# Kernel optimization log

Hardware: AMD Instinct MI355X
Metric: run time of the kernel (lower is better)

The kernel has to match this reference:

```python
import jax
import jax.numpy as jnp
import numpy as np

VOCAB = 100      # len(vocab); embedding table has VOCAB+1 rows
EMBED = 10
MID = 100
SEQ = 550
OUT = 1


def setup_inputs() -> dict:
    key = jax.random.key(0)
    ks = jax.random.split(key, 8)
    s_ih = 1.0 / np.sqrt(MID)
    return {
        "x": jax.random.randint(ks[0], (SEQ,), 0, VOCAB + 1),
        "hidden": jnp.zeros((1, 1, MID), dtype=jnp.float32),
        "embed_table": jax.random.normal(ks[1], (VOCAB + 1, EMBED), dtype=jnp.float32),
        "w_ih": jax.random.uniform(ks[2], (3 * MID, EMBED), minval=-s_ih, maxval=s_ih, dtype=jnp.float32),
        "w_hh": jax.random.uniform(ks[3], (3 * MID, MID), minval=-s_ih, maxval=s_ih, dtype=jnp.float32),
        "b_ih": jax.random.uniform(ks[4], (3 * MID,), minval=-s_ih, maxval=s_ih, dtype=jnp.float32),
        "b_hh": jax.random.uniform(ks[5], (3 * MID,), minval=-s_ih, maxval=s_ih, dtype=jnp.float32),
        "fc_w": jax.random.uniform(ks[6], (OUT, MID), minval=-s_ih, maxval=s_ih, dtype=jnp.float32),
        "fc_b": jax.random.uniform(ks[7], (OUT,), minval=-s_ih, maxval=s_ih, dtype=jnp.float32),
    }


def reference(x, hidden, embed_table, w_ih, w_hh, b_ih, b_hh, fc_w, fc_b):
    # embedding lookup: [SEQ, EMBED]
    emb = embed_table[x]
    # precompute input-side gate projections for all timesteps: [SEQ, 3*MID]
    gi_all = emb @ w_ih.T + b_ih
    h0 = hidden[0, 0]  # [MID]

    def step(h, gi):
        gh = w_hh @ h + b_hh                      # [3*MID]
        i_r, i_z, i_n = jnp.split(gi, 3)
        h_r, h_z, h_n = jnp.split(gh, 3)
        r = jax.nn.sigmoid(i_r + h_r)
        z = jax.nn.sigmoid(i_z + h_z)
        n = jnp.tanh(i_n + r * h_n)
        h_new = (1.0 - z) * n + z * h
        return h_new, None

    h_final, _ = jax.lax.scan(step, h0, gi_all)   # h_final: [MID]
    out = jax.nn.sigmoid(jax.nn.relu(h_final) @ fc_w.T + fc_b)  # [OUT]
    return out.reshape(1, 1, OUT)
```

## Files before the change

### kernel.cpp

```cpp
#include <hip/hip_runtime.h>

#define SEQ 550
#define MID 100
#define TPB 256

typedef _Float16 half2_t __attribute__((ext_vector_type(2)));

union H2I { int i; half2_t h; ushort2 u2; };

__device__ __forceinline__ float fdot2(half2_t a, half2_t b, float c) {
    return __builtin_amdgcn_fdot2(a, b, c, false);
}
__device__ __forceinline__ float sigm(float x) { return 1.0f / (1.0f + __expf(-x)); }
__device__ __forceinline__ float tanh_f(float x) { return 1.0f - 2.0f / (__expf(2.0f * x) + 1.0f); }
__device__ __forceinline__ half2_t i2h(int v) { H2I u; u.i = v; return u.h; }

__device__ __forceinline__ float pair_sum(float x) {
    int yi = __builtin_amdgcn_update_dpp(0, __float_as_int(x), 0xB1, 0xF, 0xF, true);
    return x + __int_as_float(yi);
}

__global__ __launch_bounds__(TPB, 1) void gru_fused(
    const int*   __restrict__ x,
    const float* __restrict__ hidden,
    const float* __restrict__ embed,
    const float* __restrict__ w_ih,
    const float* __restrict__ w_hh,
    const float* __restrict__ b_ih,
    const float* __restrict__ b_hh,
    const float* __restrict__ fc_w,
    const float* __restrict__ fc_b,
    float*       __restrict__ out)
{
    __shared__ __align__(16) ushort seqbuf[SEQ * 16];
    __shared__ __align__(16) int hbuf[128];
    __shared__ float partial[MID];

    const int  tid = threadIdx.x;
    const bool act = tid < 2 * MID;
    const int  u   = tid >> 1;
    const int  p   = tid & 1;
    const int  hidx = (u < 50) ? u : u + 14;

    for (int i = tid; i < SEQ * 10; i += TPB) {
        int t = i / 10;
        int k = i - 10 * t;
        H2I c; c.h = half2_t{(_Float16)embed[x[t] * 10 + k], (_Float16)0.0f};
        seqbuf[t * 16 + (k < 6 ? k : k + 2)] = c.u2.x;
    }
    for (int i = tid; i < SEQ; i += TPB)
        *(int*)(seqbuf + i * 16 + 12) = 0;

    half2_t whh[3][25];
    half2_t wihr[3][3];
    float b0 = 0.f, b1 = 0.f, b2 = 0.f, b3 = 0.f;
    float hreg = 0.f, fcw = 0.f;

    if (act) {
        #pragma unroll
        for (int r = 0; r < 3; r++) {
            const int row = r * MID + u;
            const float2* wr = (const float2*)(w_hh + row * MID) + 25 * p;
            #pragma unroll
            for (int k = 0; k < 25; k++) {
                float2 f = wr[k];
                whh[r][k] = half2_t{(_Float16)f.x, (_Float16)f.y};
            }
            const float* wi = w_ih + row * 10 + 6 * p;
            wihr[r][0] = half2_t{(_Float16)wi[0], (_Float16)wi[1]};
            wihr[r][1] = half2_t{(_Float16)wi[2], (_Float16)wi[3]};
            if (p == 0) wihr[r][2] = half2_t{(_Float16)wi[4], (_Float16)wi[5]};
            else        wihr[r][2] = half2_t{(_Float16)0.0f, (_Float16)0.0f};
        }
        if (p == 0) {
            b0 = b_ih[u]           + b_hh[u];
            b1 = b_ih[MID + u]     + b_hh[MID + u];
            b2 = b_ih[2 * MID + u];
            b3 = b_hh[2 * MID + u];
        }
        hreg = hidden[u];
        fcw  = fc_w[u];
        if (p == 0) ((_Float16*)hbuf)[hidx] = (_Float16)hreg;
    }
    float fcb = (tid == 0) ? fc_b[0] : 0.0f;

    __syncthreads();

    #pragma unroll 1
    for (int t = 0; t < SEQ; t++) {
        if (act) {
            const int   rbase = ((t & 1) << 8) + (p << 7);
            const int4* hp4   = (const int4*)((const char*)hbuf + rbase);
            int4 q0 = hp4[0], q1 = hp4[1], q2 = hp4[2], q3 = hp4[3], q4 = hp4[4], q5 = hp4[5];
            int  qe = ((const int*)hp4)[24];
            int4 ev = *(const int4*)(seqbuf + t * 16 + p * 8);

            half2_t hh[25];
            hh[0]=i2h(q0.x);  hh[1]=i2h(q0.y);  hh[2]=i2h(q0.z);  hh[3]=i2h(q0.w);
            hh[4]=i2h(q1.x);  hh[5]=i2h(q1.y);  hh[6]=i2h(q1.z);  hh[7]=i2h(q1.w);
            hh[8]=i2h(q2.x);  hh[9]=i2h(q2.y);  hh[10]=i2h(q2.z); hh[11]=i2h(q2.w);
            hh[12]=i2h(q3.x); hh[13]=i2h(q3.y); hh[14]=i2h(q3.z); hh[15]=i2h(q3.w);
            hh[16]=i2h(q4.x); hh[17]=i2h(q4.y); hh[18]=i2h(q4.z); hh[19]=i2h(q4.w);
            hh[20]=i2h(q5.x); hh[21]=i2h(q5.y); hh[22]=i2h(q5.z); hh[23]=i2h(q5.w);
            hh[24]=i2h(qe);

            float s0 = b0, s1 = b1, s2 = b2, s3 = b3;
            #pragma unroll
            for (int k = 0; k < 25; k++) {
                s0 = fdot2(whh[0][k], hh[k], s0);
                s1 = fdot2(whh[1][k], hh[k], s1);
                s3 = fdot2(whh[2][k], hh[k], s3);
            }
            half2_t e0 = i2h(ev.x), e1 = i2h(ev.y), e2 = i2h(ev.z);
            s0 = fdot2(wihr[0][0], e0, s0); s0 = fdot2(wihr[0][1], e1, s0); s0 = fdot2(wihr[0][2], e2, s0);
            s1 = fdot2(wihr[1][0], e0, s1); s1 = fdot2(wihr[1][1], e1, s1); s1 = fdot2(wihr[1][2], e2, s1);
            s2 = fdot2(wihr[2][0], e0, s2); s2 = fdot2(wihr[2][1], e1, s2); s2 = fdot2(wihr[2][2], e2, s2);

            float ar  = pair_sum(s0);
            float az  = pair_sum(s1);
            float gin = pair_sum(s2);
            float ghn = pair_sum(s3);

            float r = sigm(ar);
            float z = sigm(az);
            float n = tanh_f(gin + r * ghn);
            hreg = n + z * (hreg - n);
            if (p == 0)
                ((_Float16*)hbuf)[(((t & 1) ^ 1) << 7) + hidx] = (_Float16)hreg;
        }
        __syncthreads();
    }

    if (act && p == 0) partial[u] = fmaxf(hreg, 0.0f) * fcw;
    __syncthreads();
    if (tid == 0) {
        float s = fcb;
        const float4* pp = (const float4*)partial;
        #pragma unroll
        for (int k = 0; k < 25; k++) {
            float4 f = pp[k];
            s += (f.x + f.y) + (f.z + f.w);
        }
        out[0] = sigm(s);
    }
}

extern "C" void kernel_launch(void* const* d_in, const int* in_sizes, int n_in,
                              void* d_out, int out_size, void* d_ws, size_t ws_size,
                              hipStream_t stream) {
    const int*   x      = (const int*)  d_in[0];
    const float* hidden = (const float*)d_in[1];
    const float* embed  = (const float*)d_in[2];
    const float* w_ih   = (const float*)d_in[3];
    const float* w_hh   = (const float*)d_in[4];
    const float* b_ih   = (const float*)d_in[5];
    const float* b_hh   = (const float*)d_in[6];
    const float* fc_w   = (const float*)d_in[7];
    const float* fc_b   = (const float*)d_in[8];
    float*       out    = (float*)d_out;

    gru_fused<<<1, TPB, 0, stream>>>(x, hidden, embed, w_ih, w_hh,
                                     b_ih, b_hh, fc_w, fc_b, out);
}
```

Measured before the change: 294.7 us.

## Rewrite GRU recurrence as single-wavefront MFMA matvec with bpermute state broadcast

Shrinks the block to one 64-lane wavefront and computes the hidden-to-hidden and input projections with 16x16x32 fp16 MFMA instructions, keeping weights resident in AGPR/VGPR registers. The hidden state is broadcast across lanes via ds_bpermute instead of through shared memory with a block-wide barrier each step. Gate results go through a small LDS buffer and each lane then updates one or two hidden units. The aim is to remove per-step __syncthreads and the long scalar fdot2 chains. In exchange it adds MFMA latency and many bpermute ops to the serial critical path.

```diff
diff --git a/kernel.cpp b/kernel.cpp
--- a/kernel.cpp
+++ b/kernel.cpp
@@ -2,11 +2,16 @@
 
 #define SEQ 550
 #define MID 100
-#define TPB 256
+#define TPB 64
 
 typedef _Float16 half2_t __attribute__((ext_vector_type(2)));
-
-union H2I { int i; half2_t h; ushort2 u2; };
+typedef _Float16 half8_t __attribute__((ext_vector_type(8)));
+typedef __fp16  fp16x2  __attribute__((ext_vector_type(2)));
+typedef float f32x4 __attribute__((ext_vector_type(4)));
+
+union H2I { int i; half2_t h; };
+union H8X { half8_t h8; half2_t h2[4]; int4 i4; };
+union PKC { fp16x2 p; half2_t h; };
 
 __device__ __forceinline__ float fdot2(half2_t a, half2_t b, float c) {
     return __builtin_amdgcn_fdot2(a, b, c, false);
@@ -14,13 +19,21 @@
 __device__ __forceinline__ float sigm(float x) { return 1.0f / (1.0f + __expf(-x)); }
 __device__ __forceinline__ float tanh_f(float x) { return 1.0f - 2.0f / (__expf(2.0f * x) + 1.0f); }
 __device__ __forceinline__ half2_t i2h(int v) { H2I u; u.i = v; return u.h; }
-
-__device__ __forceinline__ float pair_sum(float x) {
-    int yi = __builtin_amdgcn_update_dpp(0, __float_as_int(x), 0xB1, 0xF, 0xF, true);
-    return x + __int_as_float(yi);
-}
-
-__global__ __launch_bounds__(TPB, 1) void gru_fused(
+__device__ __forceinline__ float pullf(int idx, float v) {
+    return __int_as_float(__builtin_amdgcn_ds_bpermute(idx, __float_as_int(v)));
+}
+__device__ __forceinline__ half2_t pk2(float a, float b) {
+    PKC u; u.p = __builtin_amdgcn_cvt_pkrtz(a, b); return u.h;
+}
+__device__ __forceinline__ half8_t zero8() {
+    return half8_t{(_Float16)0.f, (_Float16)0.f, (_Float16)0.f, (_Float16)0.f,
+                   (_Float16)0.f, (_Float16)0.f, (_Float16)0.f, (_Float16)0.f};
+}
+
+
+__global__ __launch_bounds__(TPB, 1)
+__attribute__((amdgpu_waves_per_eu(1, 1)))
+void gru_fused(
     const int*   __restrict__ x,
     const float* __restrict__ hidden,
     const float* __restrict__ embed,
@@ -32,117 +45,207 @@
     const float* __restrict__ fc_b,
     float*       __restrict__ out)
 {
-    __shared__ __align__(16) ushort seqbuf[SEQ * 16];
-    __shared__ __align__(16) int hbuf[128];
-    __shared__ float partial[MID];
-
-    const int  tid = threadIdx.x;
-    const bool act = tid < 2 * MID;
-    const int  u   = tid >> 1;
-    const int  p   = tid & 1;
-    const int  hidx = (u < 50) ? u : u + 14;
-
-    for (int i = tid; i < SEQ * 10; i += TPB) {
-        int t = i / 10;
-        int k = i - 10 * t;
-        H2I c; c.h = half2_t{(_Float16)embed[x[t] * 10 + k], (_Float16)0.0f};
-        seqbuf[t * 16 + (k < 6 ? k : k + 2)] = c.u2.x;
-    }
-    for (int i = tid; i < SEQ; i += TPB)
-        *(int*)(seqbuf + i * 16 + 12) = 0;
-
-    half2_t whh[3][25];
-    half2_t wihr[3][3];
-    float b0 = 0.f, b1 = 0.f, b2 = 0.f, b3 = 0.f;
-    float hreg = 0.f, fcw = 0.f;
-
-    if (act) {
+    __shared__ __align__(16) int seqbuf[SEQ * 16 + 16];
+    __shared__ __align__(16) int gates[400];
+
+    const int  l  = threadIdx.x;
+    const int  m  = l & 15;
+    const int  g  = l >> 4;
+    const bool m0 = (m == 0);
+
+    for (int i = l; i < SEQ * 16 + 16; i += TPB) seqbuf[i] = 0;
+    for (int i = l; i < SEQ * 5; i += TPB) {
+        int t = i / 5, j = i - 5 * t;
+        float2 f = *(const float2*)(embed + x[t] * 10 + 2 * j);
+        H2I c; c.h = half2_t{(_Float16)f.x, (_Float16)f.y};
+        seqbuf[t * 16 + j] = c.i;
+    }
+
+    half8_t ahh[19][3];
+    #pragma unroll
+    for (int tt = 0; tt < 19; tt++) {
+        int row = 0; bool val = true;
+        if (tt < 6)       row = tt * 16 + m;
+        else if (tt < 12) row = 100 + (tt - 6) * 16 + m;
+        else if (tt < 18) row = 200 + (tt - 12) * 16 + m;
+        else {
+            if (m < 4)       row = 96 + m;
+            else if (m < 8)  row = 196 + (m - 4);
+            else if (m < 12) row = 296 + (m - 8);
+            else             val = false;
+        }
         #pragma unroll
-        for (int r = 0; r < 3; r++) {
-            const int row = r * MID + u;
-            const float2* wr = (const float2*)(w_hh + row * MID) + 25 * p;
-            #pragma unroll
-            for (int k = 0; k < 25; k++) {
-                float2 f = wr[k];
-                whh[r][k] = half2_t{(_Float16)f.x, (_Float16)f.y};
+        for (int s = 0; s < 3; s++) {
+            half8_t a = zero8();
+            if (val) {
+                const float* p = w_hh + row * MID + 32 * s + 8 * g;
+                float4 f0 = *(const float4*)p;
+                float4 f1 = *(const float4*)(p + 4);
+                a = half8_t{(_Float16)f0.x, (_Float16)f0.y, (_Float16)f0.z, (_Float16)f0.w,
+                            (_Float16)f1.x, (_Float16)f1.y, (_Float16)f1.z, (_Float16)f1.w};
             }
-            const float* wi = w_ih + row * 10 + 6 * p;
-            wihr[r][0] = half2_t{(_Float16)wi[0], (_Float16)wi[1]};
-            wihr[r][1] = half2_t{(_Float16)wi[2], (_Float16)wi[3]};
-            if (p == 0) wihr[r][2] = half2_t{(_Float16)wi[4], (_Float16)wi[5]};
-            else        wihr[r][2] = half2_t{(_Float16)0.0f, (_Float16)0.0f};
-        }
-        if (p == 0) {
-            b0 = b_ih[u]           + b_hh[u];
-            b1 = b_ih[MID + u]     + b_hh[MID + u];
-            b2 = b_ih[2 * MID + u];
-            b3 = b_hh[2 * MID + u];
-        }
-        hreg = hidden[u];
-        fcw  = fc_w[u];
-        if (p == 0) ((_Float16*)hbuf)[hidx] = (_Float16)hreg;
-    }
-    float fcb = (tid == 0) ? fc_b[0] : 0.0f;
-
-    __syncthreads();
+            ahh[tt][s] = a;
+        }
+    }
+
+    half8_t aih[13];
+    #pragma unroll
+    for (int q = 0; q < 13; q++) {
+        int row = 0; bool val = true;
+        if (q < 6)       row = q * 16 + m;
+        else if (q < 12) row = 100 + (q - 6) * 16 + m;
+        else {
+            if (m < 4)      row = 96 + m;
+            else if (m < 8) row = 196 + (m - 4);
+            else            val = false;
+        }
+        half8_t a = zero8();
+        if (val) {
+            const float* p = w_ih + row * 10;
+            if (g == 0) {
+                float2 c0 = *(const float2*)(p);
+                float2 c1 = *(const float2*)(p + 2);
+                float2 c2 = *(const float2*)(p + 4);
+                float2 c3 = *(const float2*)(p + 6);
+                a = half8_t{(_Float16)c0.x, (_Float16)c0.y, (_Float16)c1.x, (_Float16)c1.y,
+                            (_Float16)c2.x, (_Float16)c2.y, (_Float16)c3.x, (_Float16)c3.y};
+            } else if (g == 1) {
+                float2 c = *(const float2*)(p + 8);
+                a[0] = (_Float16)c.x; a[1] = (_Float16)c.y;
+            }
+        }
+        aih[q] = a;
+    }
+
+    #pragma unroll
+    for (int tt = 0; tt < 19; tt++)
+        asm volatile("" : "+a"(ahh[tt][0]), "+a"(ahh[tt][1]), "+a"(ahh[tt][2]));
+    #pragma unroll
+    for (int q = 0; q < 13; q++)
+        asm volatile("" : "+v"(aih[q]));
+
+    const int u1 = l;
+    const int u2 = (l < 36) ? 64 + l : 99;
+
+    half2_t w96r1[2], w96z1[2], w96n1[2], w96r2[2], w96z2[2], w96n2[2];
+    {
+        float4 f;
+        f = *(const float4*)(w_hh + u1 * MID + 96);
+        w96r1[0] = half2_t{(_Float16)f.x, (_Float16)f.y}; w96r1[1] = half2_t{(_Float16)f.z, (_Float16)f.w};
+        f = *(const float4*)(w_hh + (MID + u1) * MID + 96);
+        w96z1[0] = half2_t{(_Float16)f.x, (_Float16)f.y}; w96z1[1] = half2_t{(_Float16)f.z, (_Float16)f.w};
+        f = *(const float4*)(w_hh + (2 * MID + u1) * MID + 96);
+        w96n1[0] = half2_t{(_Float16)f.x, (_Float16)f.y}; w96n1[1] = half2_t{(_Float16)f.z, (_Float16)f.w};
+        f = *(const float4*)(w_hh + u2 * MID + 96);
+        w96r2[0] = half2_t{(_Float16)f.x, (_Float16)f.y}; w96r2[1] = half2_t{(_Float16)f.z, (_Float16)f.w};
+        f = *(const float4*)(w_hh + (MID + u2) * MID + 96);
+        w96z2[0] = half2_t{(_Float16)f.x, (_Float16)f.y}; w96z2[1] = half2_t{(_Float16)f.z, (_Float16)f.w};
+        f = *(const float4*)(w_hh + (2 * MID + u2) * MID + 96);
+        w96n2[0] = half2_t{(_Float16)f.x, (_Float16)f.y}; w96n2[1] = half2_t{(_Float16)f.z, (_Float16)f.w};
+    }
+    half2_t win1[5], win2[5];
+    #pragma unroll
+    for (int k = 0; k < 5; k++) {
+        float2 a = *(const float2*)(w_ih + (2 * MID + u1) * 10 + 2 * k);
+        float2 b = *(const float2*)(w_ih + (2 * MID + u2) * 10 + 2 * k);
+        win1[k] = half2_t{(_Float16)a.x, (_Float16)a.y};
+        win2[k] = half2_t{(_Float16)b.x, (_Float16)b.y};
+    }
+    const float br1  = b_ih[u1] + b_hh[u1];
+    const float bz1  = b_ih[MID + u1] + b_hh[MID + u1];
+    const float bin1 = b_ih[2 * MID + u1];
+    const float bhn1 = b_hh[2 * MID + u1];
+    const float br2  = b_ih[u2] + b_hh[u2];
+    const float bz2  = b_ih[MID + u2] + b_hh[MID + u2];
+    const float bin2 = b_ih[2 * MID + u2];
+    const float bhn2 = b_hh[2 * MID + u2];
+
+    float h1 = hidden[u1];
+    float h2 = hidden[u2];
+    const float fw1 = fc_w[u1];
+    const float fw2 = fc_w[u2];
+
+    int idxA[8], idxB[8];
+    #pragma unroll
+    for (int j = 0; j < 8; j++) { idxA[j] = (8 * g + j) * 4; idxB[j] = idxA[j] + 128; }
+
+    const f32x4 zf = {0.f, 0.f, 0.f, 0.f};
+    const float* gf = (const float*)gates;
+    int soff = 0;
 
     #pragma unroll 1
     for (int t = 0; t < SEQ; t++) {
-        if (act) {
-            const int   rbase = ((t & 1) << 8) + (p << 7);
-            const int4* hp4   = (const int4*)((const char*)hbuf + rbase);
-            int4 q0 = hp4[0], q1 = hp4[1], q2 = hp4[2], q3 = hp4[3], q4 = hp4[4], q5 = hp4[5];
-            int  qe = ((const int*)hp4)[24];
-            int4 ev = *(const int4*)(seqbuf + t * 16 + p * 8);
-
-            half2_t hh[25];
-            hh[0]=i2h(q0.x);  hh[1]=i2h(q0.y);  hh[2]=i2h(q0.z);  hh[3]=i2h(q0.w);
-            hh[4]=i2h(q1.x);  hh[5]=i2h(q1.y);  hh[6]=i2h(q1.z);  hh[7]=i2h(q1.w);
-            hh[8]=i2h(q2.x);  hh[9]=i2h(q2.y);  hh[10]=i2h(q2.z); hh[11]=i2h(q2.w);
-            hh[12]=i2h(q3.x); hh[13]=i2h(q3.y); hh[14]=i2h(q3.z); hh[15]=i2h(q3.w);
-            hh[16]=i2h(q4.x); hh[17]=i2h(q4.y); hh[18]=i2h(q4.z); hh[19]=i2h(q4.w);
-            hh[20]=i2h(q5.x); hh[21]=i2h(q5.y); hh[22]=i2h(q5.z); hh[23]=i2h(q5.w);
-            hh[24]=i2h(qe);
-
-            float s0 = b0, s1 = b1, s2 = b2, s3 = b3;
-            #pragma unroll
-            for (int k = 0; k < 25; k++) {
-                s0 = fdot2(whh[0][k], hh[k], s0);
-                s1 = fdot2(whh[1][k], hh[k], s1);
-                s3 = fdot2(whh[2][k], hh[k], s3);
+        H8X be; be.i4 = *(const int4*)(seqbuf + soff + 4 * g);
+        int4 e03 = *(const int4*)(seqbuf + soff);
+        int  e4w = seqbuf[soff + 4];
+
+        H8X b0, b1, b2;
+        #pragma unroll
+        for (int j = 0; j < 4; j++) {
+            b0.h2[j] = pk2(pullf(idxA[2 * j], h1), pullf(idxA[2 * j + 1], h1));
+            b1.h2[j] = pk2(pullf(idxB[2 * j], h1), pullf(idxB[2 * j + 1], h1));
+            b2.h2[j] = pk2(pullf(idxA[2 * j], h2), pullf(idxA[2 * j + 1], h2));
+        }
+        half2_t tv0 = pk2(pullf(128, h2), pullf(132, h2));
+        half2_t tv1 = pk2(pullf(136, h2), pullf(140, h2));
+
+        #pragma unroll
+        for (int tt = 0; tt < 19; tt++) {
+            f32x4 d;
+            if (tt < 12)
+                d = __builtin_amdgcn_mfma_f32_16x16x32_f16(aih[tt], be.h8, zf, 0, 0, 0);
+            else if (tt == 18)
+                d = __builtin_amdgcn_mfma_f32_16x16x32_f16(aih[12], be.h8, zf, 0, 0, 0);
+            else
+                d = zf;
+            d = __builtin_amdgcn_mfma_f32_16x16x32_f16(ahh[tt][0], b0.h8, d, 0, 0, 0);
+            d = __builtin_amdgcn_mfma_f32_16x16x32_f16(ahh[tt][1], b1.h8, d, 0, 0, 0);
+            d = __builtin_amdgcn_mfma_f32_16x16x32_f16(ahh[tt][2], b2.h8, d, 0, 0, 0);
+            if (m0) {
+                int boff;
+                if (tt < 6)       boff = tt * 16 + 4 * g;
+                else if (tt < 12) boff = 100 + (tt - 6) * 16 + 4 * g;
+                else if (tt < 18) boff = 200 + (tt - 12) * 16 + 4 * g;
+                else              boff = (g == 0) ? 96 : (g == 1) ? 196 : (g == 2) ? 296 : 384;
+                *(f32x4*)(gates + boff) = d;
             }
-            half2_t e0 = i2h(ev.x), e1 = i2h(ev.y), e2 = i2h(ev.z);
-            s0 = fdot2(wihr[0][0], e0, s0); s0 = fdot2(wihr[0][1], e1, s0); s0 = fdot2(wihr[0][2], e2, s0);
-            s1 = fdot2(wihr[1][0], e0, s1); s1 = fdot2(wihr[1][1], e1, s1); s1 = fdot2(wihr[1][2], e2, s1);
-            s2 = fdot2(wihr[2][0], e0, s2); s2 = fdot2(wihr[2][1], e1, s2); s2 = fdot2(wihr[2][2], e2, s2);
-
-            float ar  = pair_sum(s0);
-            float az  = pair_sum(s1);
-            float gin = pair_sum(s2);
-            float ghn = pair_sum(s3);
-
-            float r = sigm(ar);
-            float z = sigm(az);
-            float n = tanh_f(gin + r * ghn);
-            hreg = n + z * (hreg - n);
-            if (p == 0)
-                ((_Float16*)hbuf)[(((t & 1) ^ 1) << 7) + hidx] = (_Float16)hreg;
-        }
-        __syncthreads();
-    }
-
-    if (act && p == 0) partial[u] = fmaxf(hreg, 0.0f) * fcw;
-    __syncthreads();
-    if (tid == 0) {
-        float s = fcb;
-        const float4* pp = (const float4*)partial;
-        #pragma unroll
-        for (int k = 0; k < 25; k++) {
-            float4 f = pp[k];
-            s += (f.x + f.y) + (f.z + f.w);
-        }
-        out[0] = sigm(s);
-    }
+        }
+
+        float gr1 = gf[u1], gz1 = gf[100 + u1], gn1 = gf[200 + u1];
+        float gr2 = gf[u2], gz2 = gf[100 + u2], gn2 = gf[200 + u2];
+
+        half2_t ev0 = i2h(e03.x), ev1 = i2h(e03.y), ev2 = i2h(e03.z), ev3 = i2h(e03.w), ev4 = i2h(e4w);
+
+        float ar1 = br1;  ar1 = fdot2(w96r1[0], tv0, ar1); ar1 = fdot2(w96r1[1], tv1, ar1); ar1 += gr1;
+        float az1 = bz1;  az1 = fdot2(w96z1[0], tv0, az1); az1 = fdot2(w96z1[1], tv1, az1); az1 += gz1;
+        float gh1 = bhn1; gh1 = fdot2(w96n1[0], tv0, gh1); gh1 = fdot2(w96n1[1], tv1, gh1); gh1 += gn1;
+        float gi1 = bin1;
+        gi1 = fdot2(win1[0], ev0, gi1); gi1 = fdot2(win1[1], ev1, gi1); gi1 = fdot2(win1[2], ev2, gi1);
+        gi1 = fdot2(win1[3], ev3, gi1); gi1 = fdot2(win1[4], ev4, gi1);
+
+        float ar2 = br2;  ar2 = fdot2(w96r2[0], tv0, ar2); ar2 = fdot2(w96r2[1], tv1, ar2); ar2 += gr2;
+        float az2 = bz2;  az2 = fdot2(w96z2[0], tv0, az2); az2 = fdot2(w96z2[1], tv1, az2); az2 += gz2;
+        float gh2 = bhn2; gh2 = fdot2(w96n2[0], tv0, gh2); gh2 = fdot2(w96n2[1], tv1, gh2); gh2 += gn2;
+        float gi2 = bin2;
+        gi2 = fdot2(win2[0], ev0, gi2); gi2 = fdot2(win2[1], ev1, gi2); gi2 = fdot2(win2[2], ev2, gi2);
+        gi2 = fdot2(win2[3], ev3, gi2); gi2 = fdot2(win2[4], ev4, gi2);
+
+        float r1 = sigm(ar1), z1 = sigm(az1);
+        float n1 = tanh_f(gi1 + r1 * gh1);
+        h1 = n1 + z1 * (h1 - n1);
+
+        float r2 = sigm(ar2), z2 = sigm(az2);
+        float n2 = tanh_f(gi2 + r2 * gh2);
+        float h2n = n2 + z2 * (h2 - n2);
+        h2 = (l < 36) ? h2n : h2;
+
+        soff += 16;
+    }
+
+    float acc = fmaxf(h1, 0.f) * fw1 + ((l < 36) ? fmaxf(h2, 0.f) * fw2 : 0.f);
+    #pragma unroll
+    for (int k = 32; k >= 1; k >>= 1) acc += __shfl_xor(acc, k, 64);
+    if (l == 0) out[0] = sigm(acc + fc_b[0]);
 }
 
 extern "C" void kernel_launch(void* const* d_in, const int* in_sizes, int n_in,
```

After: 818.9 us. 178% more time.

## Assign one hidden unit per lane across two waves, removing pair reduction

Applied to the files above, without the earlier changes.

The GRU step is reorganised so each active lane owns a full hidden unit and holds its whole 100-wide weight rows in registers, 150 packed half2 values. The block shrinks from 256 to 128 threads, two waves each covering 50 units. This removes the cross-lane DPP pair-sum and halves the number of waves taking part in the per-step barrier. The hidden state is now written as packed half2 pairs using a DPP neighbour pull, and the dot products are split into two accumulator chains to shorten dependency latency. The trade-off is doubled per-lane FMA work and heavy register pressure, forced resident with asm barriers, with only 100 of 128 lanes doing useful work.

```diff
diff --git a/kernel.cpp b/kernel.cpp
--- a/kernel.cpp
+++ b/kernel.cpp
@@ -2,11 +2,14 @@
 
 #define SEQ 550
 #define MID 100
-#define TPB 256
+#define TPB 128
 
 typedef _Float16 half2_t __attribute__((ext_vector_type(2)));
+typedef __fp16  fp16x2  __attribute__((ext_vector_type(2)));
 
-union H2I { int i; half2_t h; ushort2 u2; };
+union H2I { int i; half2_t h; };
+union PKC { fp16x2 p; half2_t h; };
+union QI  { int4 v; int s[4]; };
 
 __device__ __forceinline__ float fdot2(half2_t a, half2_t b, float c) {
     return __builtin_amdgcn_fdot2(a, b, c, false);
@@ -14,13 +17,18 @@
 __device__ __forceinline__ float sigm(float x) { return 1.0f / (1.0f + __expf(-x)); }
 __device__ __forceinline__ float tanh_f(float x) { return 1.0f - 2.0f / (__expf(2.0f * x) + 1.0f); }
 __device__ __forceinline__ half2_t i2h(int v) { H2I u; u.i = v; return u.h; }
-
-__device__ __forceinline__ float pair_sum(float x) {
-    int yi = __builtin_amdgcn_update_dpp(0, __float_as_int(x), 0xB1, 0xF, 0xF, true);
-    return x + __int_as_float(yi);
+__device__ __forceinline__ float pull_odd(float x) {
+    int y = __builtin_amdgcn_update_dpp(0, __float_as_int(x), 0xB1, 0xF, 0xF, true);
+    return __int_as_float(y);
+}
+__device__ __forceinline__ int pk2i(float a, float b) {
+    PKC u; u.p = __builtin_amdgcn_cvt_pkrtz(a, b); H2I c; c.h = u.h; return c.i;
 }
 
-__global__ __launch_bounds__(TPB, 1) void gru_fused(
+
+__global__ __launch_bounds__(TPB, 1)
+__attribute__((amdgpu_waves_per_eu(1, 1)))
+void gru_fused(
     const int*   __restrict__ x,
     const float* __restrict__ hidden,
     const float* __restrict__ embed,
@@ -32,109 +40,121 @@
     const float* __restrict__ fc_b,
     float*       __restrict__ out)
 {
-    __shared__ __align__(16) ushort seqbuf[SEQ * 16];
-    __shared__ __align__(16) int hbuf[128];
+    __shared__ __align__(16) int seqbuf[SEQ * 8];
+    __shared__ __align__(16) int hb[2][64];
     __shared__ float partial[MID];
 
-    const int  tid = threadIdx.x;
-    const bool act = tid < 2 * MID;
-    const int  u   = tid >> 1;
-    const int  p   = tid & 1;
-    const int  hidx = (u < 50) ? u : u + 14;
+    const int tid = threadIdx.x;
+    const int w   = tid >> 6;
+    const int l   = tid & 63;
+    const int lc  = (l < 50) ? l : 49;
+    const int u   = 50 * w + lc;
 
-    for (int i = tid; i < SEQ * 10; i += TPB) {
-        int t = i / 10;
-        int k = i - 10 * t;
-        H2I c; c.h = half2_t{(_Float16)embed[x[t] * 10 + k], (_Float16)0.0f};
-        seqbuf[t * 16 + (k < 6 ? k : k + 2)] = c.u2.x;
+    for (int i = tid; i < SEQ * 5; i += TPB) {
+        int t = i / 5, j = i - 5 * t;
+        float2 f = *(const float2*)(embed + x[t] * 10 + 2 * j);
+        H2I c; c.h = half2_t{(_Float16)f.x, (_Float16)f.y};
+        seqbuf[t * 8 + j] = c.i;
     }
-    for (int i = tid; i < SEQ; i += TPB)
-        *(int*)(seqbuf + i * 16 + 12) = 0;
 
-    half2_t whh[3][25];
-    half2_t wihr[3][3];
-    float b0 = 0.f, b1 = 0.f, b2 = 0.f, b3 = 0.f;
-    float hreg = 0.f, fcw = 0.f;
+    half2_t whh[3][50];
+    half2_t wih[3][5];
+    #pragma unroll
+    for (int r = 0; r < 3; r++) {
+        const float* p = w_hh + (r * MID + u) * MID;
+        #pragma unroll
+        for (int k = 0; k < 25; k++) {
+            float4 f = ((const float4*)p)[k];
+            whh[r][2 * k]     = half2_t{(_Float16)f.x, (_Float16)f.y};
+            whh[r][2 * k + 1] = half2_t{(_Float16)f.z, (_Float16)f.w};
+        }
+        const float* q = w_ih + (r * MID + u) * 10;
+        #pragma unroll
+        for (int k = 0; k < 5; k++) {
+            float2 f = *(const float2*)(q + 2 * k);
+            wih[r][k] = half2_t{(_Float16)f.x, (_Float16)f.y};
+        }
+    }
+    #pragma unroll
+    for (int r = 0; r < 3; r++) {
+        #pragma unroll
+        for (int k = 0; k < 50; k++) asm volatile("" : "+v"(whh[r][k]));
+        #pragma unroll
+        for (int k = 0; k < 5; k++)  asm volatile("" : "+v"(wih[r][k]));
+    }
 
-    if (act) {
-        #pragma unroll
-        for (int r = 0; r < 3; r++) {
-            const int row = r * MID + u;
-            const float2* wr = (const float2*)(w_hh + row * MID) + 25 * p;
-            #pragma unroll
-            for (int k = 0; k < 25; k++) {
-                float2 f = wr[k];
-                whh[r][k] = half2_t{(_Float16)f.x, (_Float16)f.y};
-            }
-            const float* wi = w_ih + row * 10 + 6 * p;
-            wihr[r][0] = half2_t{(_Float16)wi[0], (_Float16)wi[1]};
-            wihr[r][1] = half2_t{(_Float16)wi[2], (_Float16)wi[3]};
-            if (p == 0) wihr[r][2] = half2_t{(_Float16)wi[4], (_Float16)wi[5]};
-            else        wihr[r][2] = half2_t{(_Float16)0.0f, (_Float16)0.0f};
-        }
-        if (p == 0) {
-            b0 = b_ih[u]           + b_hh[u];
-            b1 = b_ih[MID + u]     + b_hh[MID + u];
-            b2 = b_ih[2 * MID + u];
-            b3 = b_hh[2 * MID + u];
-        }
-        hreg = hidden[u];
-        fcw  = fc_w[u];
-        if (p == 0) ((_Float16*)hbuf)[hidx] = (_Float16)hreg;
+    const float br  = b_ih[u] + b_hh[u];
+    const float bz  = b_ih[MID + u] + b_hh[MID + u];
+    const float bin = b_ih[2 * MID + u];
+    const float bhn = b_hh[2 * MID + u];
+
+    float hreg = hidden[u];
+    const float fcw = fc_w[u];
+
+    {
+        float ho = pull_odd(hreg);
+        if (l < 50 && !(l & 1)) hb[0][25 * w + (l >> 1)] = pk2i(hreg, ho);
     }
-    float fcb = (tid == 0) ? fc_b[0] : 0.0f;
-
     __syncthreads();
 
     #pragma unroll 1
     for (int t = 0; t < SEQ; t++) {
-        if (act) {
-            const int   rbase = ((t & 1) << 8) + (p << 7);
-            const int4* hp4   = (const int4*)((const char*)hbuf + rbase);
-            int4 q0 = hp4[0], q1 = hp4[1], q2 = hp4[2], q3 = hp4[3], q4 = hp4[4], q5 = hp4[5];
-            int  qe = ((const int*)hp4)[24];
-            int4 ev = *(const int4*)(seqbuf + t * 16 + p * 8);
+        const int* rb = hb[t & 1];
 
-            half2_t hh[25];
-            hh[0]=i2h(q0.x);  hh[1]=i2h(q0.y);  hh[2]=i2h(q0.z);  hh[3]=i2h(q0.w);
-            hh[4]=i2h(q1.x);  hh[5]=i2h(q1.y);  hh[6]=i2h(q1.z);  hh[7]=i2h(q1.w);
-            hh[8]=i2h(q2.x);  hh[9]=i2h(q2.y);  hh[10]=i2h(q2.z); hh[11]=i2h(q2.w);
-            hh[12]=i2h(q3.x); hh[13]=i2h(q3.y); hh[14]=i2h(q3.z); hh[15]=i2h(q3.w);
-            hh[16]=i2h(q4.x); hh[17]=i2h(q4.y); hh[18]=i2h(q4.z); hh[19]=i2h(q4.w);
-            hh[20]=i2h(q5.x); hh[21]=i2h(q5.y); hh[22]=i2h(q5.z); hh[23]=i2h(q5.w);
-            hh[24]=i2h(qe);
+        const int* eb = seqbuf + t * 8;
+        int4 e4 = *(const int4*)eb;
+        int  e1 = eb[4];
 
-            float s0 = b0, s1 = b1, s2 = b2, s3 = b3;
-            #pragma unroll
-            for (int k = 0; k < 25; k++) {
-                s0 = fdot2(whh[0][k], hh[k], s0);
-                s1 = fdot2(whh[1][k], hh[k], s1);
-                s3 = fdot2(whh[2][k], hh[k], s3);
+        QI qa[12];
+        const int4* hp = (const int4*)rb;
+        #pragma unroll
+        for (int j = 0; j < 12; j++) qa[j].v = hp[j];
+        int2 qb = ((const int2*)rb)[24];
+
+        half2_t ev0 = i2h(e4.x), ev1 = i2h(e4.y), ev2 = i2h(e4.z), ev3 = i2h(e4.w), ev4 = i2h(e1);
+        float arE = 0.f, azE = 0.f, gin = bin;
+        arE = fdot2(wih[0][0], ev0, arE); arE = fdot2(wih[0][1], ev1, arE);
+        arE = fdot2(wih[0][2], ev2, arE); arE = fdot2(wih[0][3], ev3, arE);
+        arE = fdot2(wih[0][4], ev4, arE);
+        azE = fdot2(wih[1][0], ev0, azE); azE = fdot2(wih[1][1], ev1, azE);
+        azE = fdot2(wih[1][2], ev2, azE); azE = fdot2(wih[1][3], ev3, azE);
+        azE = fdot2(wih[1][4], ev4, azE);
+        gin = fdot2(wih[2][0], ev0, gin); gin = fdot2(wih[2][1], ev1, gin);
+        gin = fdot2(wih[2][2], ev2, gin); gin = fdot2(wih[2][3], ev3, gin);
+        gin = fdot2(wih[2][4], ev4, gin);
+
+        float ar = br, az = bz, ghn = bhn;
+        float ar2 = 0.f, az2 = 0.f, ghn2 = 0.f;
+        #pragma unroll
+        for (int k = 0; k < 50; k++) {
+            int raw = (k < 48) ? qa[k >> 2].s[k & 3] : ((k == 48) ? qb.x : qb.y);
+            half2_t hv = i2h(raw);
+            if (k < 25) {
+                ar   = fdot2(whh[0][k], hv, ar);
+                az   = fdot2(whh[1][k], hv, az);
+                ghn  = fdot2(whh[2][k], hv, ghn);
+            } else {
+                ar2  = fdot2(whh[0][k], hv, ar2);
+                az2  = fdot2(whh[1][k], hv, az2);
+                ghn2 = fdot2(whh[2][k], hv, ghn2);
             }
-            half2_t e0 = i2h(ev.x), e1 = i2h(ev.y), e2 = i2h(ev.z);
-            s0 = fdot2(wihr[0][0], e0, s0); s0 = fdot2(wihr[0][1], e1, s0); s0 = fdot2(wihr[0][2], e2, s0);
-            s1 = fdot2(wihr[1][0], e0, s1); s1 = fdot2(wihr[1][1], e1, s1); s1 = fdot2(wihr[1][2], e2, s1);
-            s2 = fdot2(wihr[2][0], e0, s2); s2 = fdot2(wihr[2][1], e1, s2); s2 = fdot2(wihr[2][2], e2, s2);
+        }
 
-            float ar  = pair_sum(s0);
-            float az  = pair_sum(s1);
-            float gin = pair_sum(s2);
-            float ghn = pair_sum(s3);
+        float R = sigm((ar + ar2) + arE);
+        float Z = sigm((az + az2) + azE);
+        float N = tanh_f(gin + R * (ghn + ghn2));
+        hreg = N + Z * (hreg - N);
 
-            float r = sigm(ar);
-            float z = sigm(az);
-            float n = tanh_f(gin + r * ghn);
-            hreg = n + z * (hreg - n);
-            if (p == 0)
-                ((_Float16*)hbuf)[(((t & 1) ^ 1) << 7) + hidx] = (_Float16)hreg;
-        }
+        float ho = pull_odd(hreg);
+        if (l < 50 && !(l & 1)) hb[(t & 1) ^ 1][25 * w + (l >> 1)] = pk2i(hreg, ho);
+
         __syncthreads();
     }
 
-    if (act && p == 0) partial[u] = fmaxf(hreg, 0.0f) * fcw;
+    if (l < 50) partial[u] = fmaxf(hreg, 0.f) * fcw;
     __syncthreads();
     if (tid == 0) {
-        float s = fcb;
+        float s = fc_b[0];
         const float4* pp = (const float4*)partial;
         #pragma unroll
         for (int k = 0; k < 25; k++) {
```

Result: slower. 374.6 us (+27.1%).
